# Performance work log

Hardware: AMD Instinct MI355X
Metric: run time of the kernel (lower is better)

The kernel has to match this reference:

```python
import jax, jax.numpy as jnp
import numpy as np

HID = 64; H = 2; D = 32; L = 2; G = 64; F_IN = 771
NA = 120000; NE = 60000; E0 = 1500000; E1 = 1000000; E2 = 1000000


def _seg_mean(x, seg, n):
    s = jax.ops.segment_sum(x, seg, num_segments=n)
    c = jax.ops.segment_sum(jnp.ones((x.shape[0], 1), x.dtype), seg, num_segments=n)
    return s / jnp.maximum(c, 1.0)


def setup_inputs() -> dict:
    ks = jax.random.split(jax.random.key(0), 32)
    r = lambda i, s: 0.02 * jax.random.normal(ks[i], s, jnp.float32)
    z = lambda s: jnp.zeros(s, jnp.float32)
    inp = {}
    inp['x_argument'] = jax.random.normal(ks[0], (NA, F_IN), jnp.float32)
    inp['x_evidence'] = jax.random.normal(ks[1], (NE, F_IN), jnp.float32)
    inp['Win'] = r(2, (2, F_IN, HID)); inp['b_in'] = z((2, HID))
    inp['Wk'] = r(3, (L, 2, HID, HID)); inp['bk'] = z((L, 2, HID))
    inp['Wq'] = r(4, (L, 2, HID, HID)); inp['bq'] = z((L, 2, HID))
    inp['Wv'] = r(5, (L, 2, HID, HID)); inp['bv'] = z((L, 2, HID))
    inp['Wa'] = r(6, (L, 2, HID, HID)); inp['ba'] = z((L, 2, HID))
    inp['skip'] = jnp.ones((L, 2), jnp.float32)
    inp['Watt'] = r(7, (L, 3, H, D, D)); inp['Wmsg'] = r(8, (L, 3, H, D, D))
    inp['prel'] = jnp.ones((L, 3, H), jnp.float32)
    inp['Wnews'] = r(9, (384, HID)); inp['bnews'] = z((HID,))
    inp['Wdeb'] = r(10, (HID, HID)); inp['bdeb'] = z((HID,))
    inp['Wqm'] = r(11, (HID, HID)); inp['bqm'] = z((HID,))
    inp['Wkm'] = r(12, (HID, HID)); inp['bkm'] = z((HID,))
    inp['Wvm'] = r(13, (HID, HID)); inp['bvm'] = z((HID,))
    inp['Wom'] = r(14, (HID, HID)); inp['bom'] = z((HID,))
    inp['Wc1'] = r(15, (2 * HID, 64)); inp['bc1'] = z((64,))
    inp['Wc2'] = r(16, (64, 1)); inp['bc2'] = z((1,))
    inp['e0_src'] = jax.random.randint(ks[17], (E0,), 0, NA)
    inp['e0_dst'] = jax.random.randint(ks[18], (E0,), 0, NA)
    inp['e1_src'] = jax.random.randint(ks[19], (E1,), 0, NE)
    inp['e1_dst'] = jax.random.randint(ks[20], (E1,), 0, NA)
    inp['e2_src'] = jax.random.randint(ks[21], (E2,), 0, NA)
    inp['e2_dst'] = jax.random.randint(ks[22], (E2,), 0, NE)
    inp['batch_arg'] = jnp.sort(jax.random.randint(ks[23], (NA,), 0, G))
    return inp


def reference(x_argument, x_evidence, Win, b_in, Wk, bk, Wq, bq, Wv, bv, Wa, ba,
              skip, Watt, Wmsg, prel, Wnews, bnews, Wdeb, bdeb,
              Wqm, bqm, Wkm, bkm, Wvm, bvm, Wom, bom, Wc1, bc1, Wc2, bc2,
              e0_src, e0_dst, e1_src, e1_dst, e2_src, e2_dst, batch_arg):
    # Claim embedding from RAW features (slice 384:768), pooled per graph.
    claim_raw = _seg_mean(x_argument[:, 384:768], batch_arg, G)
    # Per-node-type input projection + ReLU. type 0 = argument, 1 = evidence.
    xs = [jax.nn.relu(x_argument @ Win[0] + b_in[0]),
          jax.nn.relu(x_evidence @ Win[1] + b_in[1])]
    # (src_type, dst_type, src_idx, dst_idx) for each heterogeneous edge type.
    edges = [(0, 0, e0_src, e0_dst), (1, 0, e1_src, e1_dst), (0, 1, e2_src, e2_dst)]
    scale = 1.0 / jnp.sqrt(jnp.float32(D))
    for l in range(L):  # HGTConv stack
        Kt = [(xs[t] @ Wk[l, t] + bk[l, t]).reshape(-1, H, D) for t in range(2)]
        Qt = [(xs[t] @ Wq[l, t] + bq[l, t]).reshape(-1, H, D) for t in range(2)]
        Vt = [(xs[t] @ Wv[l, t] + bv[l, t]).reshape(-1, H, D) for t in range(2)]
        buf = {0: [], 1: []}
        for e, (s, d, src, dst) in enumerate(edges):
            k2 = jnp.einsum('ehd,hdf->ehf', Kt[s][src], Watt[l, e])  # relation key transform
            v2 = jnp.einsum('ehd,hdf->ehf', Vt[s][src], Wmsg[l, e])  # relation msg transform
            sc = (Qt[d][dst] * k2).sum(-1) * prel[l, e] * scale      # (E, H)
            buf[d].append((sc, dst, v2))
        new_xs = []
        for d in range(2):
            n = xs[d].shape[0]
            sc = jnp.concatenate([b[0] for b in buf[d]], 0)
            dst = jnp.concatenate([b[1] for b in buf[d]], 0)
            v2 = jnp.concatenate([b[2] for b in buf[d]], 0)
            # segment softmax over all incoming edges of each destination node
            m = jax.ops.segment_max(sc, dst, num_segments=n)
            ex = jnp.exp(sc - m[dst])
            den = jax.ops.segment_sum(ex, dst, num_segments=n)
            alpha = ex / den[dst]
            agg = jax.ops.segment_sum(alpha[..., None] * v2, dst, num_segments=n).reshape(n, HID)
            out = jax.nn.gelu(agg, approximate=False) @ Wa[l, d] + ba[l, d]
            beta = jax.nn.sigmoid(skip[l, d])
            new_xs.append(beta * out + (1.0 - beta) * xs[d])
        xs = new_xs
    graph_emb = _seg_mean(xs[0], batch_arg, G)
    eF = claim_raw @ Wnews + bnews          # (G, HID)
    g = graph_emb @ Wdeb + bdeb             # (G, HID)
    # MultiheadAttention with query len 1 and key len 1: softmax over a single
    # key is identically 1, so attn_out == out_proj(v_proj(g)) exactly
    # (Wqm/bqm/Wkm/bkm receive exactly zero gradient, matching torch).
    v = g @ Wvm + bvm
    attn_out = v @ Wom + bom
    h = jax.nn.relu(jnp.concatenate([g, attn_out], -1) @ Wc1 + bc1)  # dropout is eval-mode identity
    return h @ Wc2 + bc2  # (G, 1)
```

## Files before the change

kernel.cpp:

```cpp
#include <hip/hip_runtime.h>
#include <math.h>

#define N0 120000
#define N1 60000
#define E0N 1500000
#define E1N 1000000
#define E2N 1000000
#define FIN 771
#define NG 64
#define KSTEPS_IN 25

#define GB0 ((N0 + 127) / 128)
#define GB1 ((N1 + 127) / 128)
#define AB0 ((N0 + 3) / 4)
#define AB1 ((N1 + 3) / 4)
#define SB0 ((N0 + 1023) / 1024)
#define SB1 ((N1 + 1023) / 1024)
#define PREPB 70

#define Q0O   ((size_t)0)
#define KV00O ((size_t)N0 * 64)
#define KV02O ((size_t)N0 * 192)
#define Q1O   ((size_t)N0 * 320)
#define KV11O ((size_t)N0 * 320 + (size_t)N1 * 64)

typedef __attribute__((ext_vector_type(8))) short short8;
typedef __attribute__((ext_vector_type(4))) float f32x4;
typedef float f32x4u __attribute__((ext_vector_type(4), aligned(4)));
typedef __attribute__((ext_vector_type(4))) unsigned short ushort4v;
typedef unsigned short ushort;

__device__ __forceinline__ float gelu_f(float v) {
    return 0.5f * v * (1.f + erff(v * 0.70710678118654752f));
}
__device__ __forceinline__ ushort f2b(float f) {
    union { float f; unsigned u; } v; v.f = f;
    unsigned u = v.u;
    return (ushort)((u + 0x7FFFu + ((u >> 16) & 1u)) >> 16);
}
__device__ __forceinline__ float lo16(unsigned u) {
    union { unsigned x; float f; } v; v.x = u << 16; return v.f;
}
__device__ __forceinline__ float hi16(unsigned u) {
    union { unsigned x; float f; } v; v.x = u & 0xFFFF0000u; return v.f;
}
__device__ __forceinline__ int asi(float f) { union { float f; int i; } v; v.f = f; return v.i; }
__device__ __forceinline__ float asf(int i) { union { int i; float f; } v; v.i = i; return v.f; }

__device__ __forceinline__ void proj_phase(
    const ushort* xls, int type, int l, int w, int lane, int r0, int nrows,
    const ushort* __restrict__ Wpack, const float* __restrict__ bpack,
    ushort* __restrict__ projAll)
{
    short8 bfr[2][2];
    #pragma unroll
    for (int ksp = 0; ksp < 2; ++ksp)
        #pragma unroll
        for (int rb = 0; rb < 2; ++rb)
            bfr[ksp][rb] = *(const short8*)&xls[(w * 32 + rb * 16 + (lane & 15)) * 72
                                                + ksp * 32 + (lane >> 4) * 8];
    const int nslots = type ? 3 : 5;
    const int sbase = l * 8 + (type ? 5 : 0);
    const int c0b = (lane >> 4) * 4;

    for (int slot = 0; slot < nslots; ++slot) {
        const ushort* Wp = Wpack + (size_t)(sbase + slot) * 4096;
        const float* bias = bpack + (size_t)(sbase + slot) * 64;
        size_t ooff; unsigned pitch, qs, ph;
        if (slot == 0) { ooff = type ? Q1O : Q0O; pitch = 64; qs = 4; ph = 0; }
        else {
            int kv = (slot + 1) >> 1;
            ooff = type ? KV11O : (kv == 1 ? KV00O : KV02O);
            pitch = 128; qs = 8; ph = (slot & 1) ? 0u : 4u;
        }
        ushort* out = projAll + ooff;
        f32x4 acc[2][4] = {};
        #pragma unroll
        for (int ksp = 0; ksp < 2; ++ksp) {
            const ushort* wb = Wp + ksp * 2048 + lane * 8;
            #pragma unroll
            for (int cg = 0; cg < 4; ++cg) {
                short8 afr = *(const short8*)&wb[cg * 512];
                acc[0][cg] = __builtin_amdgcn_mfma_f32_16x16x32_bf16(afr, bfr[ksp][0], acc[0][cg], 0, 0, 0);
                acc[1][cg] = __builtin_amdgcn_mfma_f32_16x16x32_bf16(afr, bfr[ksp][1], acc[1][cg], 0, 0, 0);
            }
        }
        #pragma unroll
        for (int rb = 0; rb < 2; ++rb) {
            int r = r0 + rb * 16 + (lane & 15);
            if (r < nrows) {
                #pragma unroll
                for (int cg = 0; cg < 4; ++cg) {
                    int c = cg * 16 + c0b;
                    ushort4v o;
                    o[0] = f2b(acc[rb][cg][0] + bias[c + 0]);
                    o[1] = f2b(acc[rb][cg][1] + bias[c + 1]);
                    o[2] = f2b(acc[rb][cg][2] + bias[c + 2]);
                    o[3] = f2b(acc[rb][cg][3] + bias[c + 3]);
                    *(ushort4v*)&out[(size_t)r * pitch + (unsigned)(c >> 2) * qs + ph] = o;
                }
            }
        }
    }
}

__global__ __launch_bounds__(256) void inproj_proj_kernel(
    const float* __restrict__ xa, const float* __restrict__ xe,
    const ushort* __restrict__ Wpin, const float* __restrict__ b_in,
    float* __restrict__ xs0, float* __restrict__ xs1,
    const ushort* __restrict__ Wpack, const float* __restrict__ bpack,
    ushort* __restrict__ projAll)
{
    __shared__ ushort xls[128 * 72];
    const int bx = blockIdx.x;
    const int type = (bx >= GB0) ? 1 : 0;
    const float* __restrict__ x = type ? xe : xa;
    const int nrows = type ? N1 : N0;
    const ushort* __restrict__ Wp = Wpin + (type ? (size_t)KSTEPS_IN * 2048 : 0);
    const float* __restrict__ bias = b_in + type * 64;
    float* __restrict__ out = type ? xs1 : xs0;

    const int tid = threadIdx.x, w = tid >> 6, lane = tid & 63;
    const int r0b = (type ? bx - GB0 : bx) * 128;
    const int r0 = r0b + w * 32;

    const int rA = min(r0 + (lane & 15), nrows - 1);
    const int rB = min(r0 + 16 + (lane & 15), nrows - 1);
    const float* __restrict__ xA = x + (size_t)rA * FIN + (lane >> 4) * 8;
    const float* __restrict__ xB = x + (size_t)rB * FIN + (lane >> 4) * 8;

    f32x4 acc[2][4] = {};
    f32x4u cb[3][4];
    cb[0][0] = *(const f32x4u*)xA;        cb[0][1] = *(const f32x4u*)(xA + 4);
    cb[0][2] = *(const f32x4u*)xB;        cb[0][3] = *(const f32x4u*)(xB + 4);
    cb[1][0] = *(const f32x4u*)(xA + 32); cb[1][1] = *(const f32x4u*)(xA + 36);
    cb[1][2] = *(const f32x4u*)(xB + 32); cb[1][3] = *(const f32x4u*)(xB + 36);

    #pragma unroll
    for (int ks = 0; ks < 24; ++ks) {
        if (ks + 2 < 24) {
            const float* pA = xA + (ks + 2) * 32;
            const float* pB = xB + (ks + 2) * 32;
            cb[(ks + 2) % 3][0] = *(const f32x4u*)pA;
            cb[(ks + 2) % 3][1] = *(const f32x4u*)(pA + 4);
            cb[(ks + 2) % 3][2] = *(const f32x4u*)pB;
            cb[(ks + 2) % 3][3] = *(const f32x4u*)(pB + 4);
        }
        const int cur = ks % 3;
        short8 bA, bB;
        #pragma unroll
        for (int j = 0; j < 4; ++j) {
            bA[j]     = (short)f2b(cb[cur][0][j]);
            bA[j + 4] = (short)f2b(cb[cur][1][j]);
            bB[j]     = (short)f2b(cb[cur][2][j]);
            bB[j + 4] = (short)f2b(cb[cur][3][j]);
        }
        const ushort* wb = Wp + (size_t)ks * 2048 + lane * 8;
        #pragma unroll
        for (int cg = 0; cg < 4; ++cg) {
            short8 afr = *(const short8*)&wb[cg * 512];
            acc[0][cg] = __builtin_amdgcn_mfma_f32_16x16x32_bf16(afr, bA, acc[0][cg], 0, 0, 0);
            acc[1][cg] = __builtin_amdgcn_mfma_f32_16x16x32_bf16(afr, bB, acc[1][cg], 0, 0, 0);
        }
    }
    {
        short8 bA = {}, bB = {};
        if ((lane >> 4) == 0) {
            const float* tA = x + (size_t)rA * FIN + 768;
            const float* tB = x + (size_t)rB * FIN + 768;
            bA[0] = (short)f2b(tA[0]); bA[1] = (short)f2b(tA[1]); bA[2] = (short)f2b(tA[2]);
            bB[0] = (short)f2b(tB[0]); bB[1] = (short)f2b(tB[1]); bB[2] = (short)f2b(tB[2]);
        }
        const ushort* wb = Wp + (size_t)24 * 2048 + lane * 8;
        #pragma unroll
        for (int cg = 0; cg < 4; ++cg) {
            short8 afr = *(const short8*)&wb[cg * 512];
            acc[0][cg] = __builtin_amdgcn_mfma_f32_16x16x32_bf16(afr, bA, acc[0][cg], 0, 0, 0);
            acc[1][cg] = __builtin_amdgcn_mfma_f32_16x16x32_bf16(afr, bB, acc[1][cg], 0, 0, 0);
        }
    }
    const int c0b = (lane >> 4) * 4;
    #pragma unroll
    for (int rb = 0; rb < 2; ++rb) {
        int lrow = w * 32 + rb * 16 + (lane & 15);
        int r = r0b + lrow;
        #pragma unroll
        for (int cg = 0; cg < 4; ++cg) {
            int c = cg * 16 + c0b;
            float4 o;
            o.x = fmaxf(acc[rb][cg][0] + bias[c + 0], 0.f);
            o.y = fmaxf(acc[rb][cg][1] + bias[c + 1], 0.f);
            o.z = fmaxf(acc[rb][cg][2] + bias[c + 2], 0.f);
            o.w = fmaxf(acc[rb][cg][3] + bias[c + 3], 0.f);
            ushort4v h;
            h[0] = f2b(o.x); h[1] = f2b(o.y); h[2] = f2b(o.z); h[3] = f2b(o.w);
            *(ushort4v*)&xls[lrow * 72 + c] = h;
            if (r < nrows) *(float4*)&out[(size_t)r * 64 + c] = o;
        }
    }
    __syncthreads();
    proj_phase(xls, type, 0, w, lane, r0, nrows, Wpack, bpack, projAll);
}

template <int DO_PROJ>
__global__ __launch_bounds__(256) void epi_kernel(
    const float* __restrict__ agg0, const float* __restrict__ agg1,
    const ushort* __restrict__ WaPack, const float* __restrict__ ba,
    float* __restrict__ xs0, float* __restrict__ xs1,
    const float* __restrict__ skip, int l,
    const ushort* __restrict__ Wpack, const float* __restrict__ bpack,
    ushort* __restrict__ projAll)
{
    __shared__ ushort xls[DO_PROJ ? 128 * 72 : 64];
    const int bx = blockIdx.x;
    const int type = (bx >= GB0) ? 1 : 0;
    const float* __restrict__ in = type ? agg1 : agg0;
    float* __restrict__ xs = type ? xs1 : xs0;
    const int nrows = type ? N1 : N0;
    const ushort* __restrict__ Wp = WaPack + (size_t)(l * 2 + type) * 4096;
    const float* __restrict__ bias = ba + (size_t)(l * 2 + type) * 64;
    const float beta = 1.f / (1.f + __expf(-skip[l * 2 + type]));

    const int tid = threadIdx.x, w = tid >> 6, lane = tid & 63;
    const int r0b = (type ? bx - GB0 : bx) * 128;
    const int r0 = r0b + w * 32;
    f32x4 acc[2][4] = {};
    #pragma unroll
    for (int ksp = 0; ksp < 2; ++ksp) {
        short8 bfr[2];
        #pragma unroll
        for (int rb = 0; rb < 2; ++rb) {
            int gr = min(r0 + rb * 16 + (lane & 15), nrows - 1);
            const float* src = in + (size_t)gr * 64 + ksp * 32 + (lane >> 4) * 8;
            float4 f0 = *(const float4*)src;
            float4 f1 = *(const float4*)(src + 4);
            short8 t;
            t[0] = (short)f2b(gelu_f(f0.x)); t[1] = (short)f2b(gelu_f(f0.y));
            t[2] = (short)f2b(gelu_f(f0.z)); t[3] = (short)f2b(gelu_f(f0.w));
            t[4] = (short)f2b(gelu_f(f1.x)); t[5] = (short)f2b(gelu_f(f1.y));
            t[6] = (short)f2b(gelu_f(f1.z)); t[7] = (short)f2b(gelu_f(f1.w));
            bfr[rb] = t;
        }
        const ushort* wb = Wp + ksp * 2048 + lane * 8;
        #pragma unroll
        for (int cg = 0; cg < 4; ++cg) {
            short8 afr = *(const short8*)&wb[cg * 512];
            acc[0][cg] = __builtin_amdgcn_mfma_f32_16x16x32_bf16(afr, bfr[0], acc[0][cg], 0, 0, 0);
            acc[1][cg] = __builtin_amdgcn_mfma_f32_16x16x32_bf16(afr, bfr[1], acc[1][cg], 0, 0, 0);
        }
    }
    const int c0b = (lane >> 4) * 4;
    #pragma unroll
    for (int rb = 0; rb < 2; ++rb) {
        int lrow = w * 32 + rb * 16 + (lane & 15);
        int r = r0b + lrow;
        int gr = min(r, nrows - 1);
        #pragma unroll
        for (int cg = 0; cg < 4; ++cg) {
            int c = cg * 16 + c0b;
            float4 xo = *(const float4*)&xs[(size_t)gr * 64 + c];
            float4 o;
            o.x = beta * (acc[rb][cg][0] + bias[c + 0]) + (1.f - beta) * xo.x;
            o.y = beta * (acc[rb][cg][1] + bias[c + 1]) + (1.f - beta) * xo.y;
            o.z = beta * (acc[rb][cg][2] + bias[c + 2]) + (1.f - beta) * xo.z;
            o.w = beta * (acc[rb][cg][3] + bias[c + 3]) + (1.f - beta) * xo.w;
            if (DO_PROJ) {
                ushort4v h;
                h[0] = f2b(o.x); h[1] = f2b(o.y); h[2] = f2b(o.z); h[3] = f2b(o.w);
                *(ushort4v*)&xls[lrow * 72 + c] = h;
            }
            if (r < nrows) *(float4*)&xs[(size_t)r * 64 + c] = o;
        }
    }
    if (DO_PROJ) {
        __syncthreads();
        proj_phase(xls, type, l + 1, w, lane, r0, nrows, Wpack, bpack, projAll);
    }
}

__global__ __launch_bounds__(256) void prep_zero_kernel(
    const float* __restrict__ Wq, const float* __restrict__ bq,
    const float* __restrict__ Wk, const float* __restrict__ bk,
    const float* __restrict__ Wv, const float* __restrict__ bv,
    const float* __restrict__ Watt, const float* __restrict__ Wmsg,
    const float* __restrict__ prel, const float* __restrict__ Win,
    const float* __restrict__ Wa,
    ushort* __restrict__ Wpack, float* __restrict__ bpack,
    ushort* __restrict__ Wpin, ushort* __restrict__ WaPack,
    int* __restrict__ c0, int* __restrict__ c1,
    int* __restrict__ gs, int* __restrict__ gc)
{
    __shared__ float WF[4096];
    const int b = blockIdx.x;
    const int tid = threadIdx.x;
    if (b >= PREPB) {
        int i = (b - PREPB) * 256 + tid;
        if (i < N0) c0[i] = 0;
        else if (i < N0 + N1) c1[i - N0] = 0;
        else if (i < N0 + N1 + NG * 64) gs[i - N0 - N1] = 0;
        else if (i < N0 + N1 + NG * 64 + NG) gc[i - N0 - N1 - NG * 64] = 0;
        return;
    }
    if (b < 16) {
        const int l = b >> 3;
        const int slot = b & 7;
        const float SCALE = 0.17677669529663689f;
        ushort* outW = Wpack + (size_t)(l * 8 + slot) * 4096;
        float* outB = bpack + (size_t)(l * 8 + slot) * 64;
        const float *Wsrc = 0, *bsrc = 0, *A = 0, *prelE = 0;
        int copy = 0;
        switch (slot) {
            case 0: Wsrc = Wq + (l*2+0)*4096; bsrc = bq + (l*2+0)*64; copy = 1; break;
            case 5: Wsrc = Wq + (l*2+1)*4096; bsrc = bq + (l*2+1)*64; copy = 1; break;
            case 1: Wsrc = Wk + (l*2+0)*4096; bsrc = bk + (l*2+0)*64; A = Watt + (l*3+0)*2048; prelE = prel + l*6 + 0; break;
            case 2: Wsrc = Wv + (l*2+0)*4096; bsrc = bv + (l*2+0)*64; A = Wmsg + (l*3+0)*2048; break;
            case 3: Wsrc = Wk + (l*2+0)*4096; bsrc = bk + (l*2+0)*64; A = Watt + (l*3+2)*2048; prelE = prel + l*6 + 4; break;
            case 4: Wsrc = Wv + (l*2+0)*4096; bsrc = bv + (l*2+0)*64; A = Wmsg + (l*3+2)*2048; break;
            case 6: Wsrc = Wk + (l*2+1)*4096; bsrc = bk + (l*2+1)*64; A = Watt + (l*3+1)*2048; prelE = prel + l*6 + 2; break;
            case 7: Wsrc = Wv + (l*2+1)*4096; bsrc = bv + (l*2+1)*64; A = Wmsg + (l*3+1)*2048; break;
        }
        if (copy) {
            for (int idx = tid; idx < 4096; idx += 256) WF[idx] = Wsrc[idx];
            if (tid < 64) outB[tid] = bsrc[tid];
        } else {
            for (int idx = tid; idx < 4096; idx += 256) {
                int k = idx >> 6, c = idx & 63, h = c >> 5, f = c & 31;
                float s = 0.f;
                for (int d = 0; d < 32; ++d)
                    s += Wsrc[k * 64 + h * 32 + d] * A[(h * 32 + d) * 32 + f];
                if (prelE) s *= prelE[h] * SCALE;
                WF[idx] = s;
            }
            if (tid < 64) {
                int h = tid >> 5, f = tid & 31;
                float s = 0.f;
                for (int d = 0; d < 32; ++d)
                    s += bsrc[h * 32 + d] * A[(h * 32 + d) * 32 + f];
                if (prelE) s *= prelE[h] * SCALE;
                outB[tid] = s;
            }
        }
        __syncthreads();
        for (int idx = tid; idx < 4096; idx += 256) {
            int ksp = idx >> 11, rem = idx & 2047;
            int cg = rem >> 9, rem2 = rem & 511;
            int lane = rem2 >> 3, j = rem2 & 7;
            int k = ksp * 32 + (lane >> 4) * 8 + j;
            int c = cg * 16 + (lane & 15);
            outW[idx] = f2b(WF[k * 64 + c]);
        }
    } else if (b < 16 + 2 * KSTEPS_IN) {
        const int pb = b - 16;
        const int type = pb / KSTEPS_IN, ks = pb % KSTEPS_IN;
        const float* W = Win + (size_t)type * FIN * 64;
        ushort* out = Wpin + (size_t)pb * 2048;
        for (int idx = tid; idx < 2048; idx += 256) {
            int cg = idx >> 9, rem = idx & 511, lane = rem >> 3, j = rem & 7;
            int k = ks * 32 + (lane >> 4) * 8 + j;
            int c = cg * 16 + (lane & 15);
            out[idx] = f2b((k < FIN) ? W[(size_t)k * 64 + c] : 0.f);
        }
    } else {
        const int mb = b - 16 - 2 * KSTEPS_IN;
        const float* W = Wa + (size_t)mb * 4096;
        ushort* o = WaPack + (size_t)mb * 4096;
        for (int idx = tid; idx < 4096; idx += 256) {
            int ksp = idx >> 11, rem = idx & 2047;
            int cg = rem >> 9, rem2 = rem & 511;
            int lane = rem2 >> 3, j = rem2 & 7;
            int k = ksp * 32 + (lane >> 4) * 8 + j;
            int c = cg * 16 + (lane & 15);
            o[idx] = f2b(W[k * 64 + c]);
        }
    }
}

__global__ void hist_all_kernel(
    const int* __restrict__ e0d, const int* __restrict__ e1d, const int* __restrict__ e2d,
    int* __restrict__ cnt0, int* __restrict__ cnt1)
{
    const int total = E0N + E1N + E2N;
    for (int i = blockIdx.x * blockDim.x + threadIdx.x; i < total; i += gridDim.x * blockDim.x) {
        if (i < E0N) atomicAdd(&cnt0[e0d[i]], 1);
        else if (i < E0N + E1N) atomicAdd(&cnt0[e1d[i - E0N]], 1);
        else atomicAdd(&cnt1[e2d[i - E0N - E1N]], 1);
    }
}

__global__ __launch_bounds__(256) void scan1_all_kernel(
    int* __restrict__ cnt0, int* __restrict__ cnt1,
    int* __restrict__ off0, int* __restrict__ off1,
    int* __restrict__ bsA, int* __restrict__ bsB)
{
    __shared__ int sa[256], sb[256];
    const int tid = threadIdx.x;
    const int b = blockIdx.x;
    int* cnt; int n; int* off; int* bsum; int lb;
    if (b < SB0) { cnt = cnt0; n = N0; off = off0; bsum = bsA; lb = b; }
    else { cnt = cnt1; n = N1; off = off1; bsum = bsB; lb = b - SB0; }
    const int base = lb * 1024 + tid * 4;
    int v[4];
    int run = 0;
    #pragma unroll
    for (int i = 0; i < 4; ++i) {
        int x = (base + i < n) ? cnt[base + i] : 0;
        run += x; v[i] = run;
    }
    #pragma unroll
    for (int i = 0; i < 4; ++i)
        if (base + i < n) cnt[base + i] = 0;
    sa[tid] = run;
    __syncthreads();
    int* src = sa; int* dst = sb;
    for (int d = 1; d < 256; d <<= 1) {
        int x = src[tid];
        if (tid >= d) x += src[tid - d];
        dst[tid] = x;
        __syncthreads();
        int* t = src; src = dst; dst = t;
    }
    int excl = src[tid] - run;
    #pragma unroll
    for (int i = 0; i < 4; ++i)
        if (base + i < n) off[base + i + 1] = excl + v[i];
    if (tid == 255) bsum[lb] = src[255];
}

__global__ __launch_bounds__(256) void scan2_all_kernel(int* __restrict__ bsA, int* __restrict__ bsB)
{
    __shared__ int sa[256], sb[256];
    const int tid = threadIdx.x;
    int* bsum = blockIdx.x ? bsB : bsA;
    const int nb = blockIdx.x ? SB1 : SB0;
    int x = (tid < nb) ? bsum[tid] : 0;
    sa[tid] = x;
    __syncthreads();
    int* src = sa; int* dst = sb;
    for (int d = 1; d < 256; d <<= 1) {
        int y = src[tid];
        if (tid >= d) y += src[tid - d];
        dst[tid] = y;
        __syncthreads();
        int* t = src; src = dst; dst = t;
    }
    if (tid < nb) bsum[tid] = src[tid] - x;
}

__global__ __launch_bounds__(256) void scan3_all_kernel(
    int* __restrict__ off0, int* __restrict__ off1,
    const int* __restrict__ bsA, const int* __restrict__ bsB)
{
    const int b = blockIdx.x;
    int* off; const int* boff; int n; int lb;
    if (b < SB0) { off = off0; boff = bsA; n = N0; lb = b; }
    else { off = off1; boff = bsB; n = N1; lb = b - SB0; }
    const int base = lb * 1024 + threadIdx.x * 4;
    const int add = boff[lb];
    #pragma unroll
    for (int i = 0; i < 4; ++i)
        if (base + i < n) off[base + i + 1] += add;
    if (lb == 0 && threadIdx.x == 0) off[0] = 0;
}

__global__ void scatter_all_kernel(
    const int* __restrict__ e0s, const int* __restrict__ e0d,
    const int* __restrict__ e1s, const int* __restrict__ e1d,
    const int* __restrict__ e2s, const int* __restrict__ e2d,
    const int* __restrict__ off0, const int* __restrict__ off1,
    int* __restrict__ cnt0, int* __restrict__ cnt1,
    int* __restrict__ rec0, int* __restrict__ rec1)
{
    const int total = E0N + E1N + E2N;
    for (int i = blockIdx.x * blockDim.x + threadIdx.x; i < total; i += gridDim.x * blockDim.x) {
        if (i < E0N) {
            int d = e0d[i];
            int pos = off0[d] + atomicAdd(&cnt0[d], 1);
            rec0[pos] = e0s[i];
        } else if (i < E0N + E1N) {
            int k = i - E0N;
            int d = e1d[k];
            int pos = off0[d] + atomicAdd(&cnt0[d], 1);
            rec0[pos] = e1s[k] | (1 << 20);
        } else {
            int k = i - E0N - E1N;
            int d = e2d[k];
            int pos = off1[d] + atomicAdd(&cnt1[d], 1);
            rec1[pos] = e2s[k];
        }
    }
}

__global__ __launch_bounds__(256) void agg_fused(
    const int* __restrict__ off0, const int* __restrict__ rec0,
    const int* __restrict__ off1, const int* __restrict__ rec1,
    const ushort* __restrict__ projAll,
    float* __restrict__ agg0, float* __restrict__ agg1)
{
    const int bx = blockIdx.x;
    const int type = (bx >= AB0) ? 1 : 0;
    const int lane = threadIdx.x & 63;
    const int node = (type ? bx - AB0 : bx) * 4 + (threadIdx.x >> 6);
    const int ndst = type ? N1 : N0;
    if (node >= ndst) return;
    const int* __restrict__ off = type ? off1 : off0;
    const int* __restrict__ rec = type ? rec1 : rec0;
    const ushort* __restrict__ Q   = projAll + (type ? Q1O : Q0O);
    const ushort* __restrict__ KVa = projAll + (type ? KV02O : KV00O);
    const ushort* __restrict__ KVb = projAll + (type ? KV02O : KV11O);
    float* __restrict__ outAgg = type ? agg1 : agg0;

    const int grp = lane >> 4;
    const int gi  = lane & 15;
    float q0, q1, q2, q3;
    {
        const unsigned* qp = (const unsigned*)(Q + (size_t)node * 64 + gi * 4);
        unsigned u0 = qp[0], u1 = qp[1];
        q0 = lo16(u0); q1 = hi16(u0); q2 = lo16(u1); q3 = hi16(u1);
    }
    const int s = off[node], e = off[node + 1];
    float den = 0.f, a0 = 0.f, a1 = 0.f, a2 = 0.f, a3 = 0.f;
    for (int j = s; j < e; j += 16) {
        bool v[4]; uint4 kv[4]; float p[4];
        #pragma unroll
        for (int q = 0; q < 4; ++q) {
            int jj = j + grp + q * 4;
            v[q] = jj < e;
            int r = rec[v[q] ? jj : s];
            const ushort* KV = (r & (1 << 20)) ? KVb : KVa;
            kv[q] = *(const uint4*)(KV + ((size_t)(unsigned)(r & 0xFFFFF) << 7) + gi * 8);
        }
        #pragma unroll
        for (int q = 0; q < 4; ++q)
            p[q] = lo16(kv[q].x) * q0 + hi16(kv[q].x) * q1 + lo16(kv[q].y) * q2 + hi16(kv[q].y) * q3;
        #pragma unroll
        for (int q = 0; q < 4; ++q) p[q] += asf(__builtin_amdgcn_ds_swizzle(asi(p[q]), 0x041F));
        #pragma unroll
        for (int q = 0; q < 4; ++q) p[q] += asf(__builtin_amdgcn_ds_swizzle(asi(p[q]), 0x081F));
        #pragma unroll
        for (int q = 0; q < 4; ++q) p[q] += asf(__builtin_amdgcn_ds_swizzle(asi(p[q]), 0x101F));
        #pragma unroll
        for (int q = 0; q < 4; ++q) {
            float wgt = v[q] ? __expf(p[q]) : 0.f;
            den += wgt;
            a0 = fmaf(wgt, lo16(kv[q].z), a0);
            a1 = fmaf(wgt, hi16(kv[q].z), a1);
            a2 = fmaf(wgt, lo16(kv[q].w), a2);
            a3 = fmaf(wgt, hi16(kv[q].w), a3);
        }
    }
    a0 += __shfl_xor(a0, 16); a0 += __shfl_xor(a0, 32);
    a1 += __shfl_xor(a1, 16); a1 += __shfl_xor(a1, 32);
    a2 += __shfl_xor(a2, 16); a2 += __shfl_xor(a2, 32);
    a3 += __shfl_xor(a3, 16); a3 += __shfl_xor(a3, 32);
    den += __shfl_xor(den, 16); den += __shfl_xor(den, 32);
    if (lane < 16) {
        float inv = (den > 0.f) ? 1.f / den : 0.f;
        float4 o;
        o.x = a0 * inv; o.y = a1 * inv; o.z = a2 * inv; o.w = a3 * inv;
        *(float4*)&outAgg[(size_t)node * 64 + gi * 4] = o;
    }
}

__global__ __launch_bounds__(256) void segsum_kernel(
    const float* __restrict__ xs, const int* __restrict__ seg, int n,
    float* __restrict__ gsum, int* __restrict__ gcnt)
{
    const int lane = threadIdx.x & 63;
    const int wid = blockIdx.x * 4 + (threadIdx.x >> 6);
    const int rbeg = wid * 256;
    if (rbeg >= n) return;
    const int rend = min(rbeg + 256, n);
    float s = 0.f;
    int cur = seg[rbeg];
    int run = 0;
    for (int r = rbeg; r < rend; ++r) {
        int sg = seg[r];
        if (sg != cur) {
            atomicAdd(&gsum[cur * 64 + lane], s);
            if (lane == 0) atomicAdd(&gcnt[cur], run);
            cur = sg; s = 0.f; run = 0;
        }
        s += xs[(size_t)r * 64 + lane];
        run++;
    }
    atomicAdd(&gsum[cur * 64 + lane], s);
    if (lane == 0) atomicAdd(&gcnt[cur], run);
}

__global__ __launch_bounds__(256) void head_kernel(
    const float* __restrict__ gsum, const int* __restrict__ gcnt,
    const float* __restrict__ Wdeb, const float* __restrict__ bdeb,
    const float* __restrict__ Wvm, const float* __restrict__ bvm,
    const float* __restrict__ Wom, const float* __restrict__ bom,
    const float* __restrict__ Wc1, const float* __restrict__ bc1,
    const float* __restrict__ Wc2, const float* __restrict__ bc2,
    float* __restrict__ outp)
{
    __shared__ float A[4096], B[4096], C[4096];
    const int tid = threadIdx.x;
    for (int idx = tid; idx < 4096; idx += 256) {
        int g = idx >> 6;
        A[idx] = gsum[idx] / fmaxf((float)gcnt[g], 1.f);
    }
    __syncthreads();
    for (int idx = tid; idx < 4096; idx += 256) {
        int g = idx >> 6, c = idx & 63;
        float s = bdeb[c];
        for (int k = 0; k < 64; ++k) s = fmaf(A[g * 64 + k], Wdeb[k * 64 + c], s);
        B[idx] = s;
    }
    __syncthreads();
    for (int idx = tid; idx < 4096; idx += 256) {
        int g = idx >> 6, c = idx & 63;
        float s = bvm[c];
        for (int k = 0; k < 64; ++k) s = fmaf(B[g * 64 + k], Wvm[k * 64 + c], s);
        C[idx] = s;
    }
    __syncthreads();
    for (int idx = tid; idx < 4096; idx += 256) {
        int g = idx >> 6, c = idx & 63;
        float s = bom[c];
        for (int k = 0; k < 64; ++k) s = fmaf(C[g * 64 + k], Wom[k * 64 + c], s);
        A[idx] = s;
    }
    __syncthreads();
    for (int idx = tid; idx < 4096; idx += 256) {
        int g = idx >> 6, c = idx & 63;
        float s = bc1[c];
        for (int k = 0; k < 64; ++k) s = fmaf(B[g * 64 + k], Wc1[k * 64 + c], s);
        for (int k = 0; k < 64; ++k) s = fmaf(A[g * 64 + k], Wc1[(64 + k) * 64 + c], s);
        C[idx] = fmaxf(s, 0.f);
    }
    __syncthreads();
    if (tid < 64) {
        float s = bc2[0];
        for (int c = 0; c < 64; ++c) s = fmaf(C[tid * 64 + c], Wc2[c], s);
        outp[tid] = s;
    }
}

extern "C" void kernel_launch(void* const* d_in, const int* in_sizes, int n_in,
                              void* d_out, int out_size, void* d_ws, size_t ws_size,
                              hipStream_t stream)
{
    const float* x_arg = (const float*)d_in[0];
    const float* x_ev  = (const float*)d_in[1];
    const float* Win   = (const float*)d_in[2];
    const float* b_in  = (const float*)d_in[3];
    const float* Wk    = (const float*)d_in[4];
    const float* bk    = (const float*)d_in[5];
    const float* Wq    = (const float*)d_in[6];
    const float* bq    = (const float*)d_in[7];
    const float* Wv    = (const float*)d_in[8];
    const float* bv    = (const float*)d_in[9];
    const float* Wa    = (const float*)d_in[10];
    const float* ba    = (const float*)d_in[11];
    const float* skip  = (const float*)d_in[12];
    const float* Watt  = (const float*)d_in[13];
    const float* Wmsg  = (const float*)d_in[14];
    const float* prel  = (const float*)d_in[15];
    const float* Wdeb  = (const float*)d_in[18];
    const float* bdeb  = (const float*)d_in[19];
    const float* Wvm   = (const float*)d_in[24];
    const float* bvm   = (const float*)d_in[25];
    const float* Wom   = (const float*)d_in[26];
    const float* bom   = (const float*)d_in[27];
    const float* Wc1   = (const float*)d_in[28];
    const float* bc1   = (const float*)d_in[29];
    const float* Wc2   = (const float*)d_in[30];
    const float* bc2   = (const float*)d_in[31];
    const int* e0s = (const int*)d_in[32];
    const int* e0d = (const int*)d_in[33];
    const int* e1s = (const int*)d_in[34];
    const int* e1d = (const int*)d_in[35];
    const int* e2s = (const int*)d_in[36];
    const int* e2d = (const int*)d_in[37];
    const int* batch = (const int*)d_in[38];
    float* outp = (float*)d_out;

    char* w = (char*)d_ws;
    size_t o = 0;
    auto alloc = [&](size_t bytes) -> char* {
        char* p = w + o;
        o = (o + bytes + 255) & ~(size_t)255;
        return p;
    };
    float* xs0   = (float*)alloc((size_t)N0 * 64 * 4);
    float* xs1   = (float*)alloc((size_t)N1 * 64 * 4);
    ushort* projAll = (ushort*)alloc(((size_t)N0 * 320 + (size_t)N1 * 192) * 2);
    float* agg0  = (float*)alloc((size_t)N0 * 64 * 4);
    float* agg1  = (float*)alloc((size_t)N1 * 64 * 4);
    int* off0 = (int*)alloc((size_t)(N0 + 1) * 4);
    int* off1 = (int*)alloc((size_t)(N1 + 1) * 4);
    int* cnt0 = (int*)alloc((size_t)N0 * 4);
    int* cnt1 = (int*)alloc((size_t)N1 * 4);
    int* rec0 = (int*)alloc((size_t)(E0N + E1N) * 4);
    int* rec1 = (int*)alloc((size_t)E2N * 4);
    int* bsA  = (int*)alloc(256 * 4);
    int* bsB  = (int*)alloc(256 * 4);
    ushort* Wpack = (ushort*)alloc((size_t)16 * 4096 * 2);
    float* bpack = (float*)alloc((size_t)16 * 64 * 4);
    ushort* Wpin = (ushort*)alloc((size_t)2 * KSTEPS_IN * 2048 * 2);
    ushort* WaPack = (ushort*)alloc((size_t)4 * 4096 * 2);
    float* gsum = (float*)alloc((size_t)NG * 64 * 4);
    int* gcnt = (int*)alloc((size_t)NG * 4);
    if (o > ws_size) return;

    const int ZB = (N0 + N1 + NG * 64 + NG + 255) / 256;

    prep_zero_kernel<<<PREPB + ZB, 256, 0, stream>>>(
        Wq, bq, Wk, bk, Wv, bv, Watt, Wmsg, prel, Win, Wa,
        Wpack, bpack, Wpin, WaPack, cnt0, cnt1, (int*)gsum, gcnt);
    hist_all_kernel<<<1280, 256, 0, stream>>>(e0d, e1d, e2d, cnt0, cnt1);
    scan1_all_kernel<<<SB0 + SB1, 256, 0, stream>>>(cnt0, cnt1, off0, off1, bsA, bsB);
    scan2_all_kernel<<<2, 256, 0, stream>>>(bsA, bsB);
    scan3_all_kernel<<<SB0 + SB1, 256, 0, stream>>>(off0, off1, bsA, bsB);
    scatter_all_kernel<<<1280, 256, 0, stream>>>(
        e0s, e0d, e1s, e1d, e2s, e2d, off0, off1, cnt0, cnt1, rec0, rec1);
    inproj_proj_kernel<<<GB0 + GB1, 256, 0, stream>>>(
        x_arg, x_ev, Wpin, b_in, xs0, xs1, Wpack, bpack, projAll);
    agg_fused<<<AB0 + AB1, 256, 0, stream>>>(off0, rec0, off1, rec1, projAll, agg0, agg1);
    epi_kernel<1><<<GB0 + GB1, 256, 0, stream>>>(
        agg0, agg1, WaPack, ba, xs0, xs1, skip, 0, Wpack, bpack, projAll);
    agg_fused<<<AB0 + AB1, 256, 0, stream>>>(off0, rec0, off1, rec1, projAll, agg0, agg1);
    epi_kernel<0><<<GB0 + GB1, 256, 0, stream>>>(
        agg0, agg1, WaPack, ba, xs0, xs1, skip, 1, Wpack, bpack, projAll);
    {
        int waves = (N0 + 255) / 256;
        segsum_kernel<<<(waves + 3) / 4, 256, 0, stream>>>(xs0, batch, N0, gsum, gcnt);
    }
    head_kernel<<<1, 256, 0, stream>>>(gsum, gcnt, Wdeb, bdeb, Wvm, bvm, Wom, bom,
                                       Wc1, bc1, Wc2, bc2, outp);
}
```

Baseline: 1.090 ms.

## Stage input-projection activations through LDS with async global_load_lds double buffering

The fused input-projection kernel used to load fp32 activation rows straight into registers, using a 3-deep software pipeline and a separate special-case tail step. It now has each wave issue direct global-to-LDS 16-byte loads (global_load_lds) into a two-slot LDS staging buffer. That buffer shares a union with the later bf16 tile. MFMA fragments are read from LDS and converted to bf16. The aim is to cut register pressure and get more memory-level parallelism on this bandwidth-heavy 771-wide read. In exchange it adds a block barrier every k-step and only prefetches one step ahead. The last k-step reads past column 771 into the next row, clamped at the buffer end, and relies on zero-padded packed weights to cancel that data.

```diff
diff --git a/kernel.cpp b/kernel.cpp
--- a/kernel.cpp
+++ b/kernel.cpp
@@ -26,7 +26,6 @@
 
 typedef __attribute__((ext_vector_type(8))) short short8;
 typedef __attribute__((ext_vector_type(4))) float f32x4;
-typedef float f32x4u __attribute__((ext_vector_type(4), aligned(4)));
 typedef __attribute__((ext_vector_type(4))) unsigned short ushort4v;
 typedef unsigned short ushort;
 
@@ -46,6 +45,10 @@
 }
 __device__ __forceinline__ int asi(float f) { union { float f; int i; } v; v.f = f; return v.i; }
 __device__ __forceinline__ float asf(int i) { union { int i; float f; } v; v.i = i; return v.f; }
+
+#define GLOAD_LDS16(gsrc, ldst) __builtin_amdgcn_global_load_lds( \
+    (const __attribute__((address_space(1))) void*)(gsrc),        \
+    (__attribute__((address_space(3))) void*)(ldst), 16, 0, 0)
 
 __device__ __forceinline__ void proj_phase(
     const ushort* xls, int type, int l, int w, int lane, int r0, int nrows,
@@ -111,7 +114,10 @@
     const ushort* __restrict__ Wpack, const float* __restrict__ bpack,
     ushort* __restrict__ projAll)
 {
-    __shared__ ushort xls[128 * 72];
+    __shared__ union {
+        float stage[2][4096];
+        ushort xls[128 * 72];
+    } sm;
     const int bx = blockIdx.x;
     const int type = (bx >= GB0) ? 1 : 0;
     const float* __restrict__ x = type ? xe : xa;
@@ -123,62 +129,61 @@
     const int tid = threadIdx.x, w = tid >> 6, lane = tid & 63;
     const int r0b = (type ? bx - GB0 : bx) * 128;
     const int r0 = r0b + w * 32;
-
-    const int rA = min(r0 + (lane & 15), nrows - 1);
-    const int rB = min(r0 + 16 + (lane & 15), nrows - 1);
-    const float* __restrict__ xA = x + (size_t)rA * FIN + (lane >> 4) * 8;
-    const float* __restrict__ xB = x + (size_t)rB * FIN + (lane >> 4) * 8;
+    const float* xlim = x + ((size_t)nrows * FIN - 4);
+
+    const int srow = (lane >> 3);
+    const int scol = (lane & 7) * 4;
 
     f32x4 acc[2][4] = {};
-    f32x4u cb[3][4];
-    cb[0][0] = *(const f32x4u*)xA;        cb[0][1] = *(const f32x4u*)(xA + 4);
-    cb[0][2] = *(const f32x4u*)xB;        cb[0][3] = *(const f32x4u*)(xB + 4);
-    cb[1][0] = *(const f32x4u*)(xA + 32); cb[1][1] = *(const f32x4u*)(xA + 36);
-    cb[1][2] = *(const f32x4u*)(xB + 32); cb[1][3] = *(const f32x4u*)(xB + 36);
-
-    #pragma unroll
-    for (int ks = 0; ks < 24; ++ks) {
-        if (ks + 2 < 24) {
-            const float* pA = xA + (ks + 2) * 32;
-            const float* pB = xB + (ks + 2) * 32;
-            cb[(ks + 2) % 3][0] = *(const f32x4u*)pA;
-            cb[(ks + 2) % 3][1] = *(const f32x4u*)(pA + 4);
-            cb[(ks + 2) % 3][2] = *(const f32x4u*)pB;
-            cb[(ks + 2) % 3][3] = *(const f32x4u*)(pB + 4);
-        }
-        const int cur = ks % 3;
-        short8 bA, bB;
-        #pragma unroll
-        for (int j = 0; j < 4; ++j) {
-            bA[j]     = (short)f2b(cb[cur][0][j]);
-            bA[j + 4] = (short)f2b(cb[cur][1][j]);
-            bB[j]     = (short)f2b(cb[cur][2][j]);
-            bB[j + 4] = (short)f2b(cb[cur][3][j]);
+
+    #pragma unroll
+    for (int i = 0; i < 4; ++i) {
+        int inst = w * 4 + i;
+        int grow = min(r0b + inst * 8 + srow, nrows - 1);
+        const float* src = x + (size_t)grow * FIN + scol;
+        if (src > xlim) src = xlim;
+        GLOAD_LDS16(src, &sm.stage[0][inst * 256]);
+    }
+    __syncthreads();
+
+    for (int ks = 0; ks < KSTEPS_IN; ++ks) {
+        if (ks + 1 < KSTEPS_IN) {
+            const int k0 = (ks + 1) * 32;
+            float* dbuf = sm.stage[(ks + 1) & 1];
+            #pragma unroll
+            for (int i = 0; i < 4; ++i) {
+                int inst = w * 4 + i;
+                int grow = min(r0b + inst * 8 + srow, nrows - 1);
+                const float* src = x + (size_t)grow * FIN + k0 + scol;
+                if (src > xlim) src = xlim;
+                GLOAD_LDS16(src, &dbuf[inst * 256]);
+            }
+        }
+        const float* bufc = sm.stage[ks & 1];
+        short8 bfr[2];
+        #pragma unroll
+        for (int rb = 0; rb < 2; ++rb) {
+            int row = w * 32 + rb * 16 + (lane & 15);
+            const float* p = bufc + row * 32 + (lane >> 4) * 8;
+            float4 f0 = *(const float4*)p;
+            float4 f1 = *(const float4*)(p + 4);
+            short8 t;
+            t[0] = (short)f2b(f0.x); t[1] = (short)f2b(f0.y);
+            t[2] = (short)f2b(f0.z); t[3] = (short)f2b(f0.w);
+            t[4] = (short)f2b(f1.x); t[5] = (short)f2b(f1.y);
+            t[6] = (short)f2b(f1.z); t[7] = (short)f2b(f1.w);
+            bfr[rb] = t;
         }
         const ushort* wb = Wp + (size_t)ks * 2048 + lane * 8;
         #pragma unroll
         for (int cg = 0; cg < 4; ++cg) {
             short8 afr = *(const short8*)&wb[cg * 512];
-            acc[0][cg] = __builtin_amdgcn_mfma_f32_16x16x32_bf16(afr, bA, acc[0][cg], 0, 0, 0);
-            acc[1][cg] = __builtin_amdgcn_mfma_f32_16x16x32_bf16(afr, bB, acc[1][cg], 0, 0, 0);
-        }
-    }
-    {
-        short8 bA = {}, bB = {};
-        if ((lane >> 4) == 0) {
-            const float* tA = x + (size_t)rA * FIN + 768;
-            const float* tB = x + (size_t)rB * FIN + 768;
-            bA[0] = (short)f2b(tA[0]); bA[1] = (short)f2b(tA[1]); bA[2] = (short)f2b(tA[2]);
-            bB[0] = (short)f2b(tB[0]); bB[1] = (short)f2b(tB[1]); bB[2] = (short)f2b(tB[2]);
-        }
-        const ushort* wb = Wp + (size_t)24 * 2048 + lane * 8;
-        #pragma unroll
-        for (int cg = 0; cg < 4; ++cg) {
-            short8 afr = *(const short8*)&wb[cg * 512];
-            acc[0][cg] = __builtin_amdgcn_mfma_f32_16x16x32_bf16(afr, bA, acc[0][cg], 0, 0, 0);
-            acc[1][cg] = __builtin_amdgcn_mfma_f32_16x16x32_bf16(afr, bB, acc[1][cg], 0, 0, 0);
-        }
-    }
+            acc[0][cg] = __builtin_amdgcn_mfma_f32_16x16x32_bf16(afr, bfr[0], acc[0][cg], 0, 0, 0);
+            acc[1][cg] = __builtin_amdgcn_mfma_f32_16x16x32_bf16(afr, bfr[1], acc[1][cg], 0, 0, 0);
+        }
+        __syncthreads();
+    }
+
     const int c0b = (lane >> 4) * 4;
     #pragma unroll
     for (int rb = 0; rb < 2; ++rb) {
@@ -194,12 +199,12 @@
             o.w = fmaxf(acc[rb][cg][3] + bias[c + 3], 0.f);
             ushort4v h;
             h[0] = f2b(o.x); h[1] = f2b(o.y); h[2] = f2b(o.z); h[3] = f2b(o.w);
-            *(ushort4v*)&xls[lrow * 72 + c] = h;
+            *(ushort4v*)&sm.xls[lrow * 72 + c] = h;
             if (r < nrows) *(float4*)&out[(size_t)r * 64 + c] = o;
         }
     }
     __syncthreads();
-    proj_phase(xls, type, 0, w, lane, r0, nrows, Wpack, bpack, projAll);
+    proj_phase(sm.xls, type, 0, w, lane, r0, nrows, Wpack, bpack, projAll);
 }
 
 template <int DO_PROJ>
```

Result: faster. 1.064 ms (-2.3%).

## Store K/V projections as scaled FP8 and stage projection stores through LDS

Applied to the files above, without the earlier changes.

K and V projections are now quantized to FP8 with a fixed scale of 256 instead of bf16, halving the bytes gathered per edge in the aggregation kernel. Q stays bf16 and is pre-divided by the scale, and the scale is removed again in the final normalisation. Projection outputs are first written to swizzled shared memory and then copied to global memory as coalesced 16-byte row stores, which adds barriers and 16KB of LDS per block. FP8 loses precision in the attention scores and values, and the fixed scale can saturate or underflow.

```diff
diff --git a/kernel.cpp b/kernel.cpp
--- a/kernel.cpp
+++ b/kernel.cpp
@@ -19,16 +19,21 @@
 #define PREPB 70
 
 #define Q0O   ((size_t)0)
-#define KV00O ((size_t)N0 * 64)
-#define KV02O ((size_t)N0 * 192)
-#define Q1O   ((size_t)N0 * 320)
-#define KV11O ((size_t)N0 * 320 + (size_t)N1 * 64)
+#define KV00O ((size_t)N0 * 128)
+#define KV02O ((size_t)N0 * 256)
+#define Q1O   ((size_t)N0 * 384)
+#define KV11O ((size_t)N0 * 384 + (size_t)N1 * 128)
+
+#define SKV 256.0f
+#define INV_SKV 0.00390625f
 
 typedef __attribute__((ext_vector_type(8))) short short8;
 typedef __attribute__((ext_vector_type(4))) float f32x4;
+typedef __attribute__((ext_vector_type(2))) float f32x2;
 typedef float f32x4u __attribute__((ext_vector_type(4), aligned(4)));
 typedef __attribute__((ext_vector_type(4))) unsigned short ushort4v;
 typedef unsigned short ushort;
+typedef unsigned char uchar;
 
 __device__ __forceinline__ float gelu_f(float v) {
     return 0.5f * v * (1.f + erff(v * 0.70710678118654752f));
@@ -48,9 +53,10 @@
 __device__ __forceinline__ float asf(int i) { union { int i; float f; } v; v.i = i; return v.f; }
 
 __device__ __forceinline__ void proj_phase(
-    const ushort* xls, int type, int l, int w, int lane, int r0, int nrows,
+    const ushort* xls, char* scratch, int type, int l, int w, int lane, int tid,
+    int r0b, int nrows,
     const ushort* __restrict__ Wpack, const float* __restrict__ bpack,
-    ushort* __restrict__ projAll)
+    uchar* __restrict__ projAll)
 {
     short8 bfr[2][2];
     #pragma unroll
@@ -59,48 +65,67 @@
         for (int rb = 0; rb < 2; ++rb)
             bfr[ksp][rb] = *(const short8*)&xls[(w * 32 + rb * 16 + (lane & 15)) * 72
                                                 + ksp * 32 + (lane >> 4) * 8];
-    const int nslots = type ? 3 : 5;
     const int sbase = l * 8 + (type ? 5 : 0);
     const int c0b = (lane >> 4) * 4;
-
-    for (int slot = 0; slot < nslots; ++slot) {
-        const ushort* Wp = Wpack + (size_t)(sbase + slot) * 4096;
-        const float* bias = bpack + (size_t)(sbase + slot) * 64;
-        size_t ooff; unsigned pitch, qs, ph;
-        if (slot == 0) { ooff = type ? Q1O : Q0O; pitch = 64; qs = 4; ph = 0; }
-        else {
-            int kv = (slot + 1) >> 1;
-            ooff = type ? KV11O : (kv == 1 ? KV00O : KV02O);
-            pitch = 128; qs = 8; ph = (slot & 1) ? 0u : 4u;
-        }
-        ushort* out = projAll + ooff;
-        f32x4 acc[2][4] = {};
-        #pragma unroll
-        for (int ksp = 0; ksp < 2; ++ksp) {
-            const ushort* wb = Wp + ksp * 2048 + lane * 8;
+    const int ngroups = type ? 2 : 3;
+
+    for (int grp = 0; grp < ngroups; ++grp) {
+        const int s0 = (grp == 0) ? 0 : (grp * 2 - 1);
+        const int nsl = (grp == 0) ? 1 : 2;
+        for (int si = 0; si < nsl; ++si) {
+            const int slot = s0 + si;
+            const ushort* Wp = Wpack + (size_t)(sbase + slot) * 4096;
+            const float* bias = bpack + (size_t)(sbase + slot) * 64;
+            f32x4 acc[2][4] = {};
             #pragma unroll
-            for (int cg = 0; cg < 4; ++cg) {
-                short8 afr = *(const short8*)&wb[cg * 512];
-                acc[0][cg] = __builtin_amdgcn_mfma_f32_16x16x32_bf16(afr, bfr[ksp][0], acc[0][cg], 0, 0, 0);
-                acc[1][cg] = __builtin_amdgcn_mfma_f32_16x16x32_bf16(afr, bfr[ksp][1], acc[1][cg], 0, 0, 0);
+            for (int ksp = 0; ksp < 2; ++ksp) {
+                const ushort* wb = Wp + ksp * 2048 + lane * 8;
+                #pragma unroll
+                for (int cg = 0; cg < 4; ++cg) {
+                    short8 afr = *(const short8*)&wb[cg * 512];
+                    acc[0][cg] = __builtin_amdgcn_mfma_f32_16x16x32_bf16(afr, bfr[ksp][0], acc[0][cg], 0, 0, 0);
+                    acc[1][cg] = __builtin_amdgcn_mfma_f32_16x16x32_bf16(afr, bfr[ksp][1], acc[1][cg], 0, 0, 0);
+                }
             }
-        }
-        #pragma unroll
-        for (int rb = 0; rb < 2; ++rb) {
-            int r = r0 + rb * 16 + (lane & 15);
-            if (r < nrows) {
+            #pragma unroll
+            for (int rb = 0; rb < 2; ++rb) {
+                int lrow = w * 32 + rb * 16 + (lane & 15);
+                const int sw = (lrow & 7) << 4;
                 #pragma unroll
                 for (int cg = 0; cg < 4; ++cg) {
                     int c = cg * 16 + c0b;
-                    ushort4v o;
-                    o[0] = f2b(acc[rb][cg][0] + bias[c + 0]);
-                    o[1] = f2b(acc[rb][cg][1] + bias[c + 1]);
-                    o[2] = f2b(acc[rb][cg][2] + bias[c + 2]);
-                    o[3] = f2b(acc[rb][cg][3] + bias[c + 3]);
-                    *(ushort4v*)&out[(size_t)r * pitch + (unsigned)(c >> 2) * qs + ph] = o;
+                    float v0 = acc[rb][cg][0] + bias[c + 0];
+                    float v1 = acc[rb][cg][1] + bias[c + 1];
+                    float v2 = acc[rb][cg][2] + bias[c + 2];
+                    float v3 = acc[rb][cg][3] + bias[c + 3];
+                    if (grp == 0) {
+                        ushort4v o;
+                        o[0] = f2b(v0); o[1] = f2b(v1); o[2] = f2b(v2); o[3] = f2b(v3);
+                        *(ushort4v*)(scratch + lrow * 128 + ((c * 2) ^ sw)) = o;
+                    } else {
+                        int wrd = __builtin_amdgcn_cvt_pk_fp8_f32(v0 * SKV, v1 * SKV, 0, 0);
+                        wrd = __builtin_amdgcn_cvt_pk_fp8_f32(v2 * SKV, v3 * SKV, wrd, 1);
+                        *(int*)(scratch + lrow * 128 + ((((c >> 2) << 3) + (si << 2)) ^ sw)) = wrd;
+                    }
                 }
             }
         }
+        __syncthreads();
+        size_t ooff;
+        if (grp == 0) ooff = type ? Q1O : Q0O;
+        else if (grp == 1) ooff = type ? KV11O : KV00O;
+        else ooff = KV02O;
+        char* outg = (char*)projAll + ooff + (size_t)r0b * 128;
+        #pragma unroll
+        for (int q = 0; q < 4; ++q) {
+            int off = q * 4096 + tid * 16;
+            int row = off >> 7;
+            int inner = off & 127;
+            if (r0b + row < nrows)
+                *(uint4*)(outg + off) =
+                    *(const uint4*)(scratch + row * 128 + (inner ^ ((row & 7) << 4)));
+        }
+        __syncthreads();
     }
 }
 
@@ -109,9 +134,10 @@
     const ushort* __restrict__ Wpin, const float* __restrict__ b_in,
     float* __restrict__ xs0, float* __restrict__ xs1,
     const ushort* __restrict__ Wpack, const float* __restrict__ bpack,
-    ushort* __restrict__ projAll)
+    uchar* __restrict__ projAll)
 {
     __shared__ ushort xls[128 * 72];
+    __shared__ char scratch[16384];
     const int bx = blockIdx.x;
     const int type = (bx >= GB0) ? 1 : 0;
     const float* __restrict__ x = type ? xe : xa;
@@ -122,10 +148,9 @@
 
     const int tid = threadIdx.x, w = tid >> 6, lane = tid & 63;
     const int r0b = (type ? bx - GB0 : bx) * 128;
-    const int r0 = r0b + w * 32;
-
-    const int rA = min(r0 + (lane & 15), nrows - 1);
-    const int rB = min(r0 + 16 + (lane & 15), nrows - 1);
+
+    const int rA = min(r0b + w * 32 + (lane & 15), nrows - 1);
+    const int rB = min(r0b + w * 32 + 16 + (lane & 15), nrows - 1);
     const float* __restrict__ xA = x + (size_t)rA * FIN + (lane >> 4) * 8;
     const float* __restrict__ xB = x + (size_t)rB * FIN + (lane >> 4) * 8;
 
@@ -199,7 +224,7 @@
         }
     }
     __syncthreads();
-    proj_phase(xls, type, 0, w, lane, r0, nrows, Wpack, bpack, projAll);
+    proj_phase(xls, scratch, type, 0, w, lane, tid, r0b, nrows, Wpack, bpack, projAll);
 }
 
 template <int DO_PROJ>
@@ -209,9 +234,10 @@
     float* __restrict__ xs0, float* __restrict__ xs1,
     const float* __restrict__ skip, int l,
     const ushort* __restrict__ Wpack, const float* __restrict__ bpack,
-    ushort* __restrict__ projAll)
+    uchar* __restrict__ projAll)
 {
     __shared__ ushort xls[DO_PROJ ? 128 * 72 : 64];
+    __shared__ char scratch[DO_PROJ ? 16384 : 64];
     const int bx = blockIdx.x;
     const int type = (bx >= GB0) ? 1 : 0;
     const float* __restrict__ in = type ? agg1 : agg0;
@@ -274,7 +300,7 @@
     }
     if (DO_PROJ) {
         __syncthreads();
-        proj_phase(xls, type, l + 1, w, lane, r0, nrows, Wpack, bpack, projAll);
+        proj_phase(xls, scratch, type, l + 1, w, lane, tid, r0b, nrows, Wpack, bpack, projAll);
     }
 }
 
@@ -493,7 +519,7 @@
 __global__ __launch_bounds__(256) void agg_fused(
     const int* __restrict__ off0, const int* __restrict__ rec0,
     const int* __restrict__ off1, const int* __restrict__ rec1,
-    const ushort* __restrict__ projAll,
+    const uchar* __restrict__ projAll,
     float* __restrict__ agg0, float* __restrict__ agg1)
 {
     const int bx = blockIdx.x;
@@ -504,9 +530,9 @@
     if (node >= ndst) return;
     const int* __restrict__ off = type ? off1 : off0;
     const int* __restrict__ rec = type ? rec1 : rec0;
-    const ushort* __restrict__ Q   = projAll + (type ? Q1O : Q0O);
-    const ushort* __restrict__ KVa = projAll + (type ? KV02O : KV00O);
-    const ushort* __restrict__ KVb = projAll + (type ? KV02O : KV11O);
+    const ushort* __restrict__ Q = (const ushort*)(projAll + (type ? Q1O : Q0O));
+    const uchar* __restrict__ KVa = projAll + (type ? KV02O : KV00O);
+    const uchar* __restrict__ KVb = projAll + (type ? KV02O : KV11O);
     float* __restrict__ outAgg = type ? agg1 : agg0;
 
     const int grp = lane >> 4;
@@ -515,23 +541,27 @@
     {
         const unsigned* qp = (const unsigned*)(Q + (size_t)node * 64 + gi * 4);
         unsigned u0 = qp[0], u1 = qp[1];
-        q0 = lo16(u0); q1 = hi16(u0); q2 = lo16(u1); q3 = hi16(u1);
+        q0 = lo16(u0) * INV_SKV; q1 = hi16(u0) * INV_SKV;
+        q2 = lo16(u1) * INV_SKV; q3 = hi16(u1) * INV_SKV;
     }
     const int s = off[node], e = off[node + 1];
     float den = 0.f, a0 = 0.f, a1 = 0.f, a2 = 0.f, a3 = 0.f;
     for (int j = s; j < e; j += 16) {
-        bool v[4]; uint4 kv[4]; float p[4];
+        bool v[4]; uint2 kv[4]; float p[4];
         #pragma unroll
         for (int q = 0; q < 4; ++q) {
             int jj = j + grp + q * 4;
             v[q] = jj < e;
             int r = rec[v[q] ? jj : s];
-            const ushort* KV = (r & (1 << 20)) ? KVb : KVa;
-            kv[q] = *(const uint4*)(KV + ((size_t)(unsigned)(r & 0xFFFFF) << 7) + gi * 8);
-        }
-        #pragma unroll
-        for (int q = 0; q < 4; ++q)
-            p[q] = lo16(kv[q].x) * q0 + hi16(kv[q].x) * q1 + lo16(kv[q].y) * q2 + hi16(kv[q].y) * q3;
+            const uchar* KV = (r & (1 << 20)) ? KVb : KVa;
+            kv[q] = *(const uint2*)(KV + ((size_t)(unsigned)(r & 0xFFFFF) << 7) + gi * 8);
+        }
+        #pragma unroll
+        for (int q = 0; q < 4; ++q) {
+            f32x2 kA = __builtin_amdgcn_cvt_pk_f32_fp8(kv[q].x, 0);
+            f32x2 kB = __builtin_amdgcn_cvt_pk_f32_fp8(kv[q].x, 1);
+            p[q] = kA[0] * q0 + kA[1] * q1 + kB[0] * q2 + kB[1] * q3;
+        }
         #pragma unroll
         for (int q = 0; q < 4; ++q) p[q] += asf(__builtin_amdgcn_ds_swizzle(asi(p[q]), 0x041F));
         #pragma unroll
@@ -542,10 +572,12 @@
         for (int q = 0; q < 4; ++q) {
             float wgt = v[q] ? __expf(p[q]) : 0.f;
             den += wgt;
-            a0 = fmaf(wgt, lo16(kv[q].z), a0);
-            a1 = fmaf(wgt, hi16(kv[q].z), a1);
-            a2 = fmaf(wgt, lo16(kv[q].w), a2);
-            a3 = fmaf(wgt, hi16(kv[q].w), a3);
+            f32x2 vA = __builtin_amdgcn_cvt_pk_f32_fp8(kv[q].y, 0);
+            f32x2 vB = __builtin_amdgcn_cvt_pk_f32_fp8(kv[q].y, 1);
+            a0 = fmaf(wgt, vA[0], a0);
+            a1 = fmaf(wgt, vA[1], a1);
+            a2 = fmaf(wgt, vB[0], a2);
+            a3 = fmaf(wgt, vB[1], a3);
         }
     }
     a0 += __shfl_xor(a0, 16); a0 += __shfl_xor(a0, 32);
@@ -554,7 +586,7 @@
     a3 += __shfl_xor(a3, 16); a3 += __shfl_xor(a3, 32);
     den += __shfl_xor(den, 16); den += __shfl_xor(den, 32);
     if (lane < 16) {
-        float inv = (den > 0.f) ? 1.f / den : 0.f;
+        float inv = (den > 0.f) ? 1.f / (den * SKV) : 0.f;
         float4 o;
         o.x = a0 * inv; o.y = a1 * inv; o.z = a2 * inv; o.w = a3 * inv;
         *(float4*)&outAgg[(size_t)node * 64 + gi * 4] = o;
@@ -687,7 +719,7 @@
     };
     float* xs0   = (float*)alloc((size_t)N0 * 64 * 4);
     float* xs1   = (float*)alloc((size_t)N1 * 64 * 4);
-    ushort* projAll = (ushort*)alloc(((size_t)N0 * 320 + (size_t)N1 * 192) * 2);
+    uchar* projAll = (uchar*)alloc((size_t)N0 * 384 + (size_t)N1 * 256);
     float* agg0  = (float*)alloc((size_t)N0 * 64 * 4);
     float* agg1  = (float*)alloc((size_t)N1 * 64 * 4);
     int* off0 = (int*)alloc((size_t)(N0 + 1) * 4);
```

After: 996.0 us. 1.09x faster.
